# Optimization experiments

Measured on AMD Instinct MI355X. Metric: run time of the kernel, lower is better.

## Reference

```python
import jax, jax.numpy as jnp
import numpy as np
import math

D_MODEL, D_HEAD = 1024, 64
N_HEADS = D_MODEL // D_HEAD  # 16
EPS = 1e-6

def rms_norm(x, scale, eps=EPS):
    ms = jnp.mean(x * x, axis=-1, keepdims=True)
    return x * scale * jax.lax.rsqrt(ms + eps)

def apply_rotary_emb(x, theta):
    # theta: (..., d) rotates first 2*d dims of x
    d = theta.shape[-1]
    x1, x2, x3 = x[..., :d], x[..., d:2 * d], x[..., 2 * d:]
    cos, sin = jnp.cos(theta), jnp.sin(theta)
    return jnp.concatenate([x1 * cos - x2 * sin, x2 * cos + x1 * sin, x3], axis=-1)

def make_freqs():
    d4 = D_HEAD // 4  # 16
    log_min, log_max = math.log(math.pi), math.log(10.0 * math.pi)
    f = np.exp(np.linspace(log_min, log_max, N_HEADS * d4 + 1, dtype=np.float64)[:-1])
    return jnp.asarray(f.reshape(d4, N_HEADS).T, dtype=jnp.float32)  # (n_heads, d_head//4)

def setup_inputs() -> dict:
    key = jax.random.key(0)
    ks = jax.random.split(key, 8)
    n, l = 4, 1024
    x = jax.random.normal(ks[0], (n, l, D_MODEL), jnp.float32)
    pos = jax.random.uniform(ks[1], (n, l, 2), jnp.float32)
    attn_mask = jnp.ones((1, 1, l, l), dtype=bool)
    cond = jax.random.normal(ks[2], (n, 1, D_MODEL), jnp.float32)
    norm_w = jax.random.normal(ks[3], (D_MODEL, D_MODEL), jnp.float32) * 0.02
    qkv_w = jax.random.normal(ks[4], (3 * D_MODEL, D_MODEL), jnp.float32) * (D_MODEL ** -0.5)
    qk_scale = jnp.ones((N_HEADS, 1, 1), jnp.float32)
    out_w = jax.random.normal(ks[5], (D_MODEL, D_MODEL), jnp.float32) * 0.02
    freqs = make_freqs()
    return {"x": x, "pos": pos, "attn_mask": attn_mask, "cond": cond,
            "norm_w": norm_w, "qkv_w": qkv_w, "qk_scale": qk_scale,
            "freqs": freqs, "out_w": out_w}

def reference(x, pos, attn_mask, cond, norm_w, qkv_w, qk_scale, freqs, out_w):
    n, l, d = x.shape
    # AdaRMSNorm
    h = rms_norm(x, jnp.einsum('nlc,dc->nld', cond, norm_w) + 1.0)
    # QKV projection -> (n, h, l, e)
    qkv = jnp.einsum('nld,ed->nle', h, qkv_w)
    q, k, v = jnp.split(qkv, 3, axis=-1)
    split_heads = lambda t: t.reshape(n, l, N_HEADS, D_HEAD).transpose(0, 2, 1, 3)
    q, k, v = split_heads(q), split_heads(k), split_heads(v)
    # per-head RMSNorm (scale shape (h,1,1))
    q = rms_norm(q, qk_scale)
    k = rms_norm(k, qk_scale)
    # axial RoPE: theta (n, h, l, d_head//2)
    theta = jnp.concatenate([
        pos[:, None, :, 0:1] * freqs[None, :, None, :],
        pos[:, None, :, 1:2] * freqs[None, :, None, :],
    ], axis=-1)
    q = apply_rotary_emb(q, theta)
    k = apply_rotary_emb(k, theta)
    # SDPA
    scores = jnp.einsum('nhqe,nhke->nhqk', q, k) * (D_HEAD ** -0.5)
    scores = jnp.where(attn_mask, scores, jnp.float32(-1e30))
    attn = jax.nn.softmax(scores, axis=-1)
    o = jnp.einsum('nhqk,nhke->nhqe', attn, v)
    o = o.transpose(0, 2, 1, 3).reshape(n, l, d)
    return jnp.einsum('nld,ed->nle', o, out_w)
```

## Files before the change

kernel.cpp:

```cpp
#include <hip/hip_runtime.h>

typedef short bf16x8 __attribute__((ext_vector_type(8)));
typedef float f32x4 __attribute__((ext_vector_type(4)));

__device__ __forceinline__ float bf2f(ushort u) {
  union { unsigned int i; float f; } x; x.i = ((unsigned int)u) << 16; return x.f;
}
__device__ __forceinline__ ushort f2bf(float f) {
  union { float f; unsigned int i; } x; x.f = f;
  unsigned int r = x.i + 0x7fff + ((x.i >> 16) & 1);
  return (ushort)(r >> 16);
}
__device__ __forceinline__ unsigned int cvtpk_bf16(float a, float b) {
  unsigned int r;
  asm("v_cvt_pk_bf16_f32 %0, %1, %2" : "=v"(r) : "v"(a), "v"(b));
  return r;
}

__device__ __forceinline__ f32x4 mfma16(bf16x8 a, bf16x8 b, f32x4 c) {
  return __builtin_amdgcn_mfma_f32_16x16x32_bf16(a, b, c, 0, 0, 0);
}

__device__ __forceinline__ void gload_lds16(const void* g, void* l) {
  __builtin_amdgcn_global_load_lds(
      (const __attribute__((address_space(1))) void*)g,
      (__attribute__((address_space(3))) void*)l, 16, 0, 0);
}

__global__ __launch_bounds__(256) void f2bf_vec(const float* __restrict__ in,
                                                ushort* __restrict__ out, int n4) {
  int i = blockIdx.x * 256 + threadIdx.x;
  if (i >= n4) return;
  float4 v = ((const float4*)in)[i];
  ushort4 o;
  o.x = f2bf(v.x); o.y = f2bf(v.y); o.z = f2bf(v.z); o.w = f2bf(v.w);
  ((ushort4*)out)[i] = o;
}

__global__ __launch_bounds__(256) void cond_gemv(const float* __restrict__ cond,
                                                 const float* __restrict__ nw,
                                                 float* __restrict__ sout) {
  const int w = threadIdx.x >> 6, lane = threadIdx.x & 63;
  const int idx = blockIdx.x * 4 + w;
  const int n_ = idx >> 10, d = idx & 1023;
  const float* cr = cond + n_ * 1024;
  const float* wr_ = nw + (size_t)d * 1024;
  float sum = 0.f;
#pragma unroll
  for (int c = lane; c < 1024; c += 64) sum += cr[c] * wr_[c];
#pragma unroll
  for (int off = 1; off < 64; off <<= 1) sum += __shfl_xor(sum, off);
  if (lane == 0) sout[idx] = sum + 1.0f;
}

__global__ __launch_bounds__(256) void rmsnorm_x(const float* __restrict__ x,
                                                 const float* __restrict__ s,
                                                 ushort* __restrict__ h, int L) {
  const int row = blockIdx.x;
  const int n_ = row / L;
  const int tid = threadIdx.x;
  __shared__ float red[4];
  float4 xv = ((const float4*)(x + (size_t)row * 1024))[tid];
  float ss = xv.x * xv.x + xv.y * xv.y + xv.z * xv.z + xv.w * xv.w;
#pragma unroll
  for (int off = 1; off < 64; off <<= 1) ss += __shfl_xor(ss, off);
  if ((tid & 63) == 0) red[tid >> 6] = ss;
  __syncthreads();
  float tot = red[0] + red[1] + red[2] + red[3];
  float r = rsqrtf(tot * (1.f / 1024.f) + 1e-6f);
  float4 sv = ((const float4*)(s + (size_t)n_ * 1024))[tid];
  ushort4 o;
  o.x = f2bf(xv.x * sv.x * r);
  o.y = f2bf(xv.y * sv.y * r);
  o.z = f2bf(xv.z * sv.z * r);
  o.w = f2bf(xv.w * sv.w * r);
  ((ushort4*)(h + (size_t)row * 1024))[tid] = o;
}

template <typename OT>
__global__ __launch_bounds__(256) void gemm_bt(const ushort* __restrict__ A,
                                               const ushort* __restrict__ B,
                                               OT* __restrict__ C, int M, int N,
                                               int K, int nbx) {
  __shared__ ushort As[2][128 * 32];
  __shared__ ushort Bs[2][128 * 32];
  const int tid = threadIdx.x;
  const int w = tid >> 6;
  const int lane = tid & 63;
  const int wr = w >> 1, wc = w & 1;
  const int lm = lane & 15, g = lane >> 4;
  const int qchunk = gridDim.x >> 3;
  const int swz = (blockIdx.x & 7) * qchunk + (blockIdx.x >> 3);
  const int bn = (swz % nbx) * 128;
  const int bm = (swz / nbx) * 128;
  f32x4 acc[4][4] = {};
  const int u_ = lane >> 3;
  const int pp = (lane & 7) ^ u_;
  const int srow = (u_ << 1) | (pp >> 2);
  const int scol = (pp & 3) * 8;
  const int rb = (lm >> 1) * 64 + (((((lm & 1) << 2) | g) ^ (lm >> 1)) << 3);

  auto stage = [&](int kt, int b) {
#pragma unroll
    for (int i = 0; i < 2; ++i) {
      const int c = w * 2 + i;
      gload_lds16(&A[(size_t)(bm + c * 16 + srow) * K + kt + scol],
                  &As[b][c * 512]);
      gload_lds16(&B[(size_t)(bn + c * 16 + srow) * K + kt + scol],
                  &Bs[b][c * 512]);
    }
  };

  const int NTK = K >> 5;
  stage(0, 0);
  stage(32, 1);
  for (int t = 0; t < NTK; ++t) {
    const int b = t & 1;
    if (t + 1 < NTK)
      asm volatile("s_waitcnt vmcnt(4)" ::: "memory");
    else
      asm volatile("s_waitcnt vmcnt(0)" ::: "memory");
    __builtin_amdgcn_s_barrier();
    bf16x8 af[4], bfr[4];
#pragma unroll
    for (int mi = 0; mi < 4; ++mi)
      af[mi] = *(const bf16x8*)&As[b][(wr * 4 + mi) * 512 + rb];
#pragma unroll
    for (int ni = 0; ni < 4; ++ni)
      bfr[ni] = *(const bf16x8*)&Bs[b][(wc * 4 + ni) * 512 + rb];
    asm volatile("s_waitcnt lgkmcnt(0)" ::: "memory");
    __builtin_amdgcn_sched_barrier(0);
    __builtin_amdgcn_s_barrier();
    if (t + 2 < NTK) stage((t + 2) << 5, b);
#pragma unroll
    for (int mi = 0; mi < 4; ++mi)
#pragma unroll
      for (int ni = 0; ni < 4; ++ni)
        acc[mi][ni] = mfma16(af[mi], bfr[ni], acc[mi][ni]);
  }
#pragma unroll
  for (int mi = 0; mi < 4; ++mi)
#pragma unroll
    for (int ni = 0; ni < 4; ++ni) {
      int col = bn + wc * 64 + ni * 16 + lm;
#pragma unroll
      for (int r = 0; r < 4; ++r) {
        int row = bm + wr * 64 + mi * 16 + g * 4 + r;
        float v = acc[mi][ni][r];
        if constexpr (sizeof(OT) == 2)
          C[(size_t)row * N + col] = (OT)f2bf(v);
        else
          C[(size_t)row * N + col] = (OT)v;
      }
    }
}

__global__ __launch_bounds__(256) void qkv_prep(
    const ushort* __restrict__ qkv, const float* __restrict__ pos,
    const float* __restrict__ qscale, const float* __restrict__ freqs,
    ushort* __restrict__ Qr, ushort* __restrict__ Kr, ushort* __restrict__ Vr,
    int L) {
  const int row = blockIdx.x;
  const int n_ = row / L;
  const int l = row - n_ * L;
  const int w = threadIdx.x >> 6, lane = threadIdx.x & 63;
  const float p0 = pos[row * 2 + 0], p1 = pos[row * 2 + 1];
  const int tl = lane & 31;
#pragma unroll
  for (int hi = 0; hi < 4; ++hi) {
    const int h = w * 4 + hi;
    const size_t ib = (size_t)row * 3072 + h * 64 + lane;
    float qv = bf2f(qkv[ib]);
    float kv = bf2f(qkv[ib + 1024]);
    float vv = bf2f(qkv[ib + 2048]);
    float sq = qv * qv, sk = kv * kv;
#pragma unroll
    for (int off = 1; off < 64; off <<= 1) {
      sq += __shfl_xor(sq, off);
      sk += __shfl_xor(sk, off);
    }
    const float sc = qscale[h];
    float qn = qv * sc * rsqrtf(sq * (1.f / 64.f) + 1e-6f);
    float kn = kv * sc * rsqrtf(sk * (1.f / 64.f) + 1e-6f);
    float th = ((tl < 16) ? p0 : p1) * freqs[h * 16 + (tl & 15)];
    float s_, c_;
    sincosf(th, &s_, &c_);
    float qo = __shfl_xor(qn, 32);
    float ko = __shfl_xor(kn, 32);
    float qr = (lane < 32) ? (qn * c_ - qo * s_) : (qn * c_ + qo * s_);
    float kr = (lane < 32) ? (kn * c_ - ko * s_) : (kn * c_ + ko * s_);
    const size_t ob = ((size_t)(n_ * 16 + h) * L + l) * 64 + lane;
    Qr[ob] = f2bf(qr * 0.18033688f);
    Kr[ob] = f2bf(kr);
    Vr[ob] = f2bf(vv);
  }
}

__global__ __launch_bounds__(256) void vtrans(const ushort* __restrict__ v,
                                              ushort* __restrict__ vt) {
  __shared__ ushort T[64][72];
  const int tid = threadIdx.x;
  const int nh = blockIdx.y;
  const int l0 = blockIdx.x * 64;
  const int lr = tid >> 2;
  const int d0 = (tid & 3) * 16;
  const ushort* src = v + ((size_t)nh * 1024 + l0 + lr) * 64 + d0;
  *(uint4*)&T[lr][d0] = *(const uint4*)src;
  *(uint4*)&T[lr][d0 + 8] = *(const uint4*)(src + 8);
  __syncthreads();
  const int d = tid >> 2;
  const int lc = (tid & 3) * 16;
  ushort tmp[16];
#pragma unroll
  for (int j = 0; j < 16; ++j) tmp[j] = T[lc + j][d];
  ushort* dst = vt + ((size_t)nh * 64 + d) * 1024 + l0 + lc;
  *(uint4*)dst = *(uint4*)&tmp[0];
  *(uint4*)(dst + 8) = *(uint4*)&tmp[8];
}

__global__ __launch_bounds__(256) void attn_kernel(
    const ushort* __restrict__ Q, const ushort* __restrict__ Kg,
    const ushort* __restrict__ Vtg, ushort* __restrict__ O, int L) {
  __shared__ ushort Ks[2][64 * 64];
  __shared__ ushort Vs[2][64 * 64];
  __shared__ ushort Pb[4][16 * 64];
  const int tid = threadIdx.x;
  const int w = tid >> 6, lane = tid & 63;
  const int lm = lane & 15, g = lane >> 4;
  const int swz = (blockIdx.x & 7) * 128 + (blockIdx.x >> 3);
  const int nh = swz >> 4;
  const int qt = swz & 15;
  const ushort* q = Q + (size_t)nh * L * 64;
  const ushort* k = Kg + (size_t)nh * L * 64;
  const ushort* vt = Vtg + (size_t)nh * 64 * L;
  const int qbase = qt * 64 + w * 16;
  bf16x8 qf[2];
#pragma unroll
  for (int kc = 0; kc < 2; ++kc)
    qf[kc] = *(const bf16x8*)&q[(size_t)(qbase + lm) * 64 + kc * 32 + g * 8];
  f32x4 ot[4] = {};
  float lsum = 0.f;
  const int sr = lane >> 3;
  const int ss = (lane & 7) ^ sr;

  auto stage = [&](int tt, int b) {
#pragma unroll
    for (int i = 0; i < 2; ++i) {
      const int r = w * 16 + i * 8 + sr;
      gload_lds16(&k[(size_t)(tt * 64 + r) * 64 + ss * 8],
                  &Ks[b][(w * 16 + i * 8) * 64]);
    }
#pragma unroll
    for (int i = 0; i < 2; ++i) {
      const int r = w * 16 + i * 8 + sr;
      gload_lds16(&vt[(size_t)r * L + tt * 64 + ss * 8],
                  &Vs[b][(w * 16 + i * 8) * 64]);
    }
  };

  stage(0, 0);
  __syncthreads();
  const int NT = L >> 6;
  for (int t = 0; t < NT; ++t) {
    const int cur = t & 1;
    if (t + 1 < NT) stage(t + 1, cur ^ 1);
    const ushort* ksb = &Ks[cur][0];
    f32x4 st[4] = {};
    __builtin_amdgcn_s_setprio(1);
#pragma unroll
    for (int t16 = 0; t16 < 4; ++t16) {
      const int r = t16 * 16 + lm;
#pragma unroll
      for (int kc = 0; kc < 2; ++kc) {
        bf16x8 a = *(const bf16x8*)&ksb[r * 64 + (((kc * 4 + g) ^ (lm & 7)) << 3)];
        st[t16] = mfma16(a, qf[kc], st[t16]);
      }
    }
    __builtin_amdgcn_s_setprio(0);
    float e[4][4];
#pragma unroll
    for (int t16 = 0; t16 < 4; ++t16)
#pragma unroll
      for (int r = 0; r < 4; ++r) {
        e[t16][r] = exp2f(st[t16][r]);
        lsum += e[t16][r];
      }
    ushort* pb = &Pb[w][0];
#pragma unroll
    for (int t16 = 0; t16 < 4; ++t16) {
      unsigned int lo = cvtpk_bf16(e[t16][0], e[t16][1]);
      unsigned int hi = cvtpk_bf16(e[t16][2], e[t16][3]);
      const int slot = (t16 * 2 + (g >> 1)) ^ (lm & 7);
      *(uint2*)&pb[lm * 64 + slot * 8 + (g & 1) * 4] = make_uint2(lo, hi);
    }
    asm volatile("s_waitcnt lgkmcnt(0)" ::: "memory");
    __builtin_amdgcn_sched_barrier(0);
    bf16x8 pf[2];
#pragma unroll
    for (int c = 0; c < 2; ++c)
      pf[c] = *(const bf16x8*)&pb[lm * 64 + (((c * 4 + g) ^ (lm & 7)) << 3)];
    const ushort* vsb = &Vs[cur][0];
    __builtin_amdgcn_s_setprio(1);
#pragma unroll
    for (int db = 0; db < 4; ++db) {
      const int d = db * 16 + lm;
#pragma unroll
      for (int c = 0; c < 2; ++c) {
        bf16x8 a = *(const bf16x8*)&vsb[d * 64 + (((c * 4 + g) ^ (lm & 7)) << 3)];
        ot[db] = mfma16(a, pf[c], ot[db]);
      }
    }
    __builtin_amdgcn_s_setprio(0);
    __syncthreads();
  }
  float ls = lsum;
  ls += __shfl_xor(ls, 16);
  ls += __shfl_xor(ls, 32);
  const float inv = 1.f / ls;
  const int n_ = nh >> 4, h = nh & 15;
#pragma unroll
  for (int db = 0; db < 4; ++db) {
    unsigned int lo = cvtpk_bf16(ot[db][0] * inv, ot[db][1] * inv);
    unsigned int hi = cvtpk_bf16(ot[db][2] * inv, ot[db][3] * inv);
    size_t off =
        ((size_t)(n_ * L + qbase + lm) * 1024) + h * 64 + db * 16 + g * 4;
    *(uint2*)&O[off] = make_uint2(lo, hi);
  }
}

extern "C" void kernel_launch(void* const* d_in, const int* in_sizes, int n_in,
                              void* d_out, int out_size, void* d_ws,
                              size_t ws_size, hipStream_t stream) {
  const float* x = (const float*)d_in[0];
  const float* pos = (const float*)d_in[1];
  const float* cond = (const float*)d_in[3];
  const float* norm_w = (const float*)d_in[4];
  const float* qkv_w = (const float*)d_in[5];
  const float* qk_scale = (const float*)d_in[6];
  const float* freqs = (const float*)d_in[7];
  const float* out_w = (const float*)d_in[8];
  float* out = (float*)d_out;
  const int L = 1024;

  char* wsb = (char*)d_ws;
  ushort* qkvw_bf = (ushort*)(wsb);
  ushort* outw_bf = (ushort*)(wsb + 6291456);
  float* s_cond = (float*)(wsb + 8388608);
  ushort* h_buf = (ushort*)(wsb + 8404992);
  ushort* qkv_buf = (ushort*)(wsb + 16793600);
  ushort* q_r = (ushort*)(wsb + 41959424);
  ushort* k_r = (ushort*)(wsb + 50348032);
  ushort* v_r = (ushort*)(wsb + 58736640);
  ushort* o_buf = (ushort*)(wsb + 67125248);
  ushort* vt_buf = h_buf;

  hipLaunchKernelGGL(f2bf_vec, dim3(3072), dim3(256), 0, stream, qkv_w,
                     qkvw_bf, 786432);
  hipLaunchKernelGGL(f2bf_vec, dim3(1024), dim3(256), 0, stream, out_w,
                     outw_bf, 262144);
  hipLaunchKernelGGL(cond_gemv, dim3(1024), dim3(256), 0, stream, cond, norm_w,
                     s_cond);
  hipLaunchKernelGGL(rmsnorm_x, dim3(4096), dim3(256), 0, stream, x, s_cond,
                     h_buf, L);
  hipLaunchKernelGGL(gemm_bt<ushort>, dim3(768), dim3(256), 0, stream, h_buf,
                     qkvw_bf, qkv_buf, 4096, 3072, 1024, 24);
  hipLaunchKernelGGL(qkv_prep, dim3(4096), dim3(256), 0, stream, qkv_buf, pos,
                     qk_scale, freqs, q_r, k_r, v_r, L);
  hipLaunchKernelGGL(vtrans, dim3(16, 64), dim3(256), 0, stream, v_r, vt_buf);
  hipLaunchKernelGGL(attn_kernel, dim3(1024), dim3(256), 0, stream, q_r, k_r,
                     vt_buf, o_buf, L);
  hipLaunchKernelGGL(gemm_bt<float>, dim3(256), dim3(256), 0, stream, o_buf,
                     outw_bf, out, 4096, 1024, 1024, 8);
}
```

Measured before the change: 133.0 us.

## Shrink attention blocks to 2 waves with 32-wide Q and KV tiles

Attention blocks drop from 4 waves over 64 query rows to 2 waves over 32 query rows, and KV tiles shrink from 64 to 32 keys. Grid doubles to 2048 blocks with a new swizzle and a rotation-based LDS swizzle for K, V and P. This cuts LDS per block, which should allow more resident blocks and better tail balance. In exchange, each loaded K/V tile serves only 32 queries, so global K/V traffic doubles, and twice as many barrier iterations are needed.

```diff
diff --git a/kernel.cpp b/kernel.cpp
--- a/kernel.cpp
+++ b/kernel.cpp
@@ -218,57 +218,56 @@
   *(uint4*)(dst + 8) = *(uint4*)&tmp[8];
 }
 
-__global__ __launch_bounds__(256) void attn_kernel(
+__global__ __launch_bounds__(128) void attn_kernel(
     const ushort* __restrict__ Q, const ushort* __restrict__ Kg,
     const ushort* __restrict__ Vtg, ushort* __restrict__ O, int L) {
-  __shared__ ushort Ks[2][64 * 64];
-  __shared__ ushort Vs[2][64 * 64];
-  __shared__ ushort Pb[4][16 * 64];
+  __shared__ ushort Ks[2][32 * 64];
+  __shared__ ushort Vs[2][64 * 32];
+  __shared__ ushort Pb[2][16 * 32];
   const int tid = threadIdx.x;
   const int w = tid >> 6, lane = tid & 63;
   const int lm = lane & 15, g = lane >> 4;
-  const int swz = (blockIdx.x & 7) * 128 + (blockIdx.x >> 3);
-  const int nh = swz >> 4;
-  const int qt = swz & 15;
+  const int swz = (blockIdx.x & 7) * 256 + (blockIdx.x >> 3);
+  const int nh = swz >> 5;
+  const int qt = swz & 31;
   const ushort* q = Q + (size_t)nh * L * 64;
   const ushort* k = Kg + (size_t)nh * L * 64;
   const ushort* vt = Vtg + (size_t)nh * 64 * L;
-  const int qbase = qt * 64 + w * 16;
+  const int qbase = qt * 32 + w * 16;
   bf16x8 qf[2];
 #pragma unroll
   for (int kc = 0; kc < 2; ++kc)
     qf[kc] = *(const bf16x8*)&q[(size_t)(qbase + lm) * 64 + kc * 32 + g * 8];
   f32x4 ot[4] = {};
   float lsum = 0.f;
-  const int sr = lane >> 3;
-  const int ss = (lane & 7) ^ sr;
+  const int krow = tid >> 3;
+  const int ksrc = (tid & 7) ^ (krow & 7);
+  const int vrow = tid >> 2;
+  const int vsrc = ((tid & 3) - (vrow >> 2)) & 3;
+  const int vp = (g + (lm >> 2)) & 3;
 
   auto stage = [&](int tt, int b) {
-#pragma unroll
-    for (int i = 0; i < 2; ++i) {
-      const int r = w * 16 + i * 8 + sr;
-      gload_lds16(&k[(size_t)(tt * 64 + r) * 64 + ss * 8],
-                  &Ks[b][(w * 16 + i * 8) * 64]);
-    }
-#pragma unroll
-    for (int i = 0; i < 2; ++i) {
-      const int r = w * 16 + i * 8 + sr;
-      gload_lds16(&vt[(size_t)r * L + tt * 64 + ss * 8],
-                  &Vs[b][(w * 16 + i * 8) * 64]);
-    }
+    gload_lds16(&k[(size_t)(tt * 32 + krow) * 64 + ksrc * 8],
+                &Ks[b][w * 512]);
+    gload_lds16(&k[(size_t)(tt * 32 + 16 + krow) * 64 + ksrc * 8],
+                &Ks[b][1024 + w * 512]);
+    gload_lds16(&vt[(size_t)vrow * L + tt * 32 + vsrc * 8],
+                &Vs[b][w * 512]);
+    gload_lds16(&vt[(size_t)(32 + vrow) * L + tt * 32 + vsrc * 8],
+                &Vs[b][1024 + w * 512]);
   };
 
   stage(0, 0);
   __syncthreads();
-  const int NT = L >> 6;
+  const int NT = L >> 5;
   for (int t = 0; t < NT; ++t) {
     const int cur = t & 1;
     if (t + 1 < NT) stage(t + 1, cur ^ 1);
     const ushort* ksb = &Ks[cur][0];
-    f32x4 st[4] = {};
+    f32x4 st[2] = {};
     __builtin_amdgcn_s_setprio(1);
 #pragma unroll
-    for (int t16 = 0; t16 < 4; ++t16) {
+    for (int t16 = 0; t16 < 2; ++t16) {
       const int r = t16 * 16 + lm;
 #pragma unroll
       for (int kc = 0; kc < 2; ++kc) {
@@ -277,9 +276,9 @@
       }
     }
     __builtin_amdgcn_s_setprio(0);
-    float e[4][4];
-#pragma unroll
-    for (int t16 = 0; t16 < 4; ++t16)
+    float e[2][4];
+#pragma unroll
+    for (int t16 = 0; t16 < 2; ++t16)
 #pragma unroll
       for (int r = 0; r < 4; ++r) {
         e[t16][r] = exp2f(st[t16][r]);
@@ -287,28 +286,21 @@
       }
     ushort* pb = &Pb[w][0];
 #pragma unroll
-    for (int t16 = 0; t16 < 4; ++t16) {
+    for (int t16 = 0; t16 < 2; ++t16) {
       unsigned int lo = cvtpk_bf16(e[t16][0], e[t16][1]);
       unsigned int hi = cvtpk_bf16(e[t16][2], e[t16][3]);
-      const int slot = (t16 * 2 + (g >> 1)) ^ (lm & 7);
-      *(uint2*)&pb[lm * 64 + slot * 8 + (g & 1) * 4] = make_uint2(lo, hi);
+      const int ps = (t16 * 2 + (g >> 1) + (lm >> 2)) & 3;
+      *(uint2*)&pb[lm * 32 + ps * 8 + (g & 1) * 4] = make_uint2(lo, hi);
     }
     asm volatile("s_waitcnt lgkmcnt(0)" ::: "memory");
     __builtin_amdgcn_sched_barrier(0);
-    bf16x8 pf[2];
-#pragma unroll
-    for (int c = 0; c < 2; ++c)
-      pf[c] = *(const bf16x8*)&pb[lm * 64 + (((c * 4 + g) ^ (lm & 7)) << 3)];
+    bf16x8 pf = *(const bf16x8*)&pb[lm * 32 + vp * 8];
     const ushort* vsb = &Vs[cur][0];
     __builtin_amdgcn_s_setprio(1);
 #pragma unroll
     for (int db = 0; db < 4; ++db) {
-      const int d = db * 16 + lm;
-#pragma unroll
-      for (int c = 0; c < 2; ++c) {
-        bf16x8 a = *(const bf16x8*)&vsb[d * 64 + (((c * 4 + g) ^ (lm & 7)) << 3)];
-        ot[db] = mfma16(a, pf[c], ot[db]);
-      }
+      bf16x8 a = *(const bf16x8*)&vsb[(db * 16 + lm) * 32 + vp * 8];
+      ot[db] = mfma16(a, pf, ot[db]);
     }
     __builtin_amdgcn_s_setprio(0);
     __syncthreads();
@@ -367,7 +359,7 @@
   hipLaunchKernelGGL(qkv_prep, dim3(4096), dim3(256), 0, stream, qkv_buf, pos,
                      qk_scale, freqs, q_r, k_r, v_r, L);
   hipLaunchKernelGGL(vtrans, dim3(16, 64), dim3(256), 0, stream, v_r, vt_buf);
-  hipLaunchKernelGGL(attn_kernel, dim3(1024), dim3(256), 0, stream, q_r, k_r,
+  hipLaunchKernelGGL(attn_kernel, dim3(2048), dim3(128), 0, stream, q_r, k_r,
                      vt_buf, o_buf, L);
   hipLaunchKernelGGL(gemm_bt<float>, dim3(256), dim3(256), 0, stream, o_buf,
                      outw_bf, out, 4096, 1024, 1024, 8);
```

After: 139.7 us. +5.0%, slower.
